# Performance work log

Measured on AMD Instinct MI355X. Metric: run time of the kernel, lower is better.

## Reference

```python
import jax, jax.numpy as jnp
import numpy as np

B, S, D, H = 4, 1024, 1024, 16
DH = D // H
EPS = 1e-5


def setup_inputs() -> dict:
    key = jax.random.key(0)
    ks = jax.random.split(key, 8)
    return {
        "q": jax.random.normal(ks[0], (B, S, D), jnp.float32),
        "k": jax.random.normal(ks[1], (B, S, D), jnp.float32),
        "v": jax.random.normal(ks[2], (B, S, D), jnp.float32),
        "mask": jnp.ones((B, S), jnp.float32),
        "scores": jax.random.normal(ks[3], (B, H, S, S), jnp.float32),
        "W_proj": jax.random.normal(ks[4], (D, D), jnp.float32) / np.sqrt(D),
        "W_minus": jax.random.normal(ks[5], (D, 2 * D), jnp.float32) / np.sqrt(2 * D),
        "ln_w": jnp.ones((D,), jnp.float32),
        "ln_b": jnp.zeros((D,), jnp.float32),
        "c": jnp.zeros((1,), jnp.float32),
    }


def reference(q, k, v, mask, scores, W_proj, W_minus, ln_w, ln_b, c):
    # split heads: (B,S,D) -> (B,S,H,DH)
    qh = q.reshape(B, S, H, DH)
    kh = k.reshape(B, S, H, DH)
    vh = v.reshape(B, S, H, DH)
    # scaled QK^T plus learnable-scaled residual scores
    att_scores = jnp.einsum("bqhd,bkhd->bhqk", qh, kh) / np.sqrt(DH) + c[0] * scores
    # additive mask (mask is (B, kv_len))
    att_scores = att_scores - 1e8 * (1.0 - mask)[:, None, None, :]
    att = jax.nn.softmax(att_scores, axis=-1)
    ctx = jnp.einsum("bhqk,bkhd->bqhd", att, vh).reshape(B, S, D)
    # proj (bias-free linear); dropout is identity at inference
    x = ctx @ W_proj.T
    # concat -> minus linear -> LayerNorm
    cat = jnp.concatenate([q, x], axis=-1)
    y = cat @ W_minus.T
    mu = jnp.mean(y, axis=-1, keepdims=True)
    var = jnp.mean((y - mu) ** 2, axis=-1, keepdims=True)
    y = (y - mu) * jax.lax.rsqrt(var + EPS) * ln_w + ln_b
    return (y, att_scores)
```

## Files before the change

### kernel.cpp

```cpp
#include <hip/hip_runtime.h>
#include <hip/hip_bf16.h>
#include <math.h>

#define BB 4
#define SS 1024
#define DD 1024
#define HH 16
#define DHH 64
#define BHH (BB * HH)

#define LDB 88
#define LDC 68

typedef __attribute__((ext_vector_type(8))) short short8;
typedef __attribute__((ext_vector_type(4))) float f32x4;

__device__ __forceinline__ unsigned short f2bf(float x) {
  __hip_bfloat16 h = __float2bfloat16(x);
  return *reinterpret_cast<unsigned short*>(&h);
}

__device__ __forceinline__ void stageb(const unsigned short* __restrict__ src, int ld,
                                       unsigned short* __restrict__ dst, int tid) {
#pragma unroll
  for (int u = 0; u < 2; ++u) {
    int cidx = tid + 256 * u;
    int r = cidx >> 3;
    int c8 = (cidx & 7) * 8;
    float4 v = *reinterpret_cast<const float4*>(src + (size_t)r * ld + c8);
    *reinterpret_cast<float4*>(dst + r * LDB + c8) = v;
  }
}

__device__ __forceinline__ short8 ldfrag(const unsigned short* __restrict__ base,
                                         int row16, int kh, int lane) {
  const unsigned short* p = base + (size_t)(row16 + (lane & 15)) * LDB + kh + (lane >> 4) * 8;
  return *reinterpret_cast<const short8*>(p);
}

__device__ __forceinline__ void mfma_tile(const unsigned short* As, const unsigned short* Bs,
                                          int w, int lane, f32x4 acc[4]) {
#pragma unroll
  for (int kh = 0; kh < 64; kh += 32) {
    short8 b = ldfrag(Bs, w * 16, kh, lane);
#pragma unroll
    for (int mb = 0; mb < 4; ++mb) {
      short8 a = ldfrag(As, mb * 16, kh, lane);
      acc[mb] = __builtin_amdgcn_mfma_f32_16x16x32_bf16(a, b, acc[mb], 0, 0, 0);
    }
  }
}

__device__ __forceinline__ void acc_to_lds(float* Cs, const f32x4 acc[4], int w, int lane,
                                           float scale) {
  int quad = lane >> 4, col = w * 16 + (lane & 15);
#pragma unroll
  for (int mb = 0; mb < 4; ++mb)
#pragma unroll
    for (int r = 0; r < 4; ++r)
      Cs[(mb * 16 + quad * 4 + r) * LDC + col] = acc[mb][r] * scale;
}

__global__ __launch_bounds__(256) void cvt_kernel(const float* __restrict__ in,
                                                  unsigned short* __restrict__ out, int n4) {
  int i = blockIdx.x * 256 + threadIdx.x;
  if (i < n4) {
    float4 v = reinterpret_cast<const float4*>(in)[i];
    ushort4 o;
    o.x = f2bf(v.x); o.y = f2bf(v.y); o.z = f2bf(v.z); o.w = f2bf(v.w);
    reinterpret_cast<ushort4*>(out)[i] = o;
  }
}

__global__ __launch_bounds__(256) void vtrans_kernel(const float* __restrict__ v,
                                                     unsigned short* __restrict__ vT) {
  __shared__ unsigned short T[64 * LDC];
  int tid = threadIdx.x;
  int s0 = blockIdx.x * 64, bh = blockIdx.y;
  int b = bh >> 4, h = bh & 15;
#pragma unroll
  for (int u = 0; u < 4; ++u) {
    int f = tid + 256 * u;
    int r = f >> 4, c4 = (f & 15) * 4;
    float4 vv = *reinterpret_cast<const float4*>(v + ((size_t)(b * SS + s0 + r)) * DD + h * DHH + c4);
    T[(c4 + 0) * LDC + r] = f2bf(vv.x);
    T[(c4 + 1) * LDC + r] = f2bf(vv.y);
    T[(c4 + 2) * LDC + r] = f2bf(vv.z);
    T[(c4 + 3) * LDC + r] = f2bf(vv.w);
  }
  __syncthreads();
#pragma unroll
  for (int u = 0; u < 4; ++u) {
    int f = tid + 256 * u;
    int d = f >> 4, s4 = (f & 15) * 4;
    ushort4 o = *reinterpret_cast<const ushort4*>(&T[d * LDC + s4]);
    *reinterpret_cast<ushort4*>(vT + ((size_t)(bh * DHH + d)) * SS + s0 + s4) = o;
  }
}

__global__ __launch_bounds__(256) void qk_mfma_kernel(
    const unsigned short* __restrict__ qb, const unsigned short* __restrict__ kb,
    const float* __restrict__ scores, const float* __restrict__ mask,
    const float* __restrict__ c, float* __restrict__ att,
    float* __restrict__ pmax, float* __restrict__ psum) {
  __shared__ unsigned short smem[2 * 64 * LDB];
  unsigned short* As = smem;
  unsigned short* Bs = smem + 64 * LDB;
  float* Cs = reinterpret_cast<float*>(smem);
  int tid = threadIdx.x, lane = tid & 63, w = tid >> 6;
  int kt = blockIdx.x, qt = blockIdx.y, bh = blockIdx.z;
  int b = bh >> 4, h = bh & 15;
  int qr0 = qt * 64, kr0 = kt * 64;

  stageb(qb + ((size_t)(b * SS + qr0)) * DD + h * DHH, DD, As, tid);
  stageb(kb + ((size_t)(b * SS + kr0)) * DD + h * DHH, DD, Bs, tid);
  __syncthreads();
  f32x4 acc[4] = {};
  mfma_tile(As, Bs, w, lane, acc);
  __syncthreads();
  acc_to_lds(Cs, acc, w, lane, 0.125f);
  __syncthreads();

  float cc = c[0];
#pragma unroll
  for (int u = 0; u < 4; ++u) {
    int f = tid + 256 * u;
    int row = f >> 4, c4 = (f & 15) * 4;
    int rg = bh * SS + qr0 + row;
    size_t goff = (size_t)rg * SS + kr0 + c4;
    float4 qk = *reinterpret_cast<const float4*>(&Cs[row * LDC + c4]);
    float4 sc = *reinterpret_cast<const float4*>(scores + goff);
    float4 mv = *reinterpret_cast<const float4*>(mask + b * SS + kr0 + c4);
    float o0 = qk.x + cc * sc.x - 1e8f * (1.0f - mv.x);
    float o1 = qk.y + cc * sc.y - 1e8f * (1.0f - mv.y);
    float o2 = qk.z + cc * sc.z - 1e8f * (1.0f - mv.z);
    float o3 = qk.w + cc * sc.w - 1e8f * (1.0f - mv.w);
    float4 ov = {o0, o1, o2, o3};
    *reinterpret_cast<float4*>(att + goff) = ov;
    float m = fmaxf(fmaxf(o0, o1), fmaxf(o2, o3));
#pragma unroll
    for (int off = 1; off <= 8; off <<= 1) m = fmaxf(m, __shfl_xor(m, off));
    float l = __expf(o0 - m) + __expf(o1 - m) + __expf(o2 - m) + __expf(o3 - m);
#pragma unroll
    for (int off = 1; off <= 8; off <<= 1) l += __shfl_xor(l, off);
    if ((tid & 15) == 0) {
      pmax[(size_t)rg * 16 + kt] = m;
      psum[(size_t)rg * 16 + kt] = l;
    }
  }
}

__global__ __launch_bounds__(256) void stats_reduce_kernel(
    const float* __restrict__ pmax, const float* __restrict__ psum,
    float* __restrict__ rowm, float* __restrict__ rowinvl) {
  int idx = blockIdx.x * 256 + threadIdx.x;
  const float* pm = pmax + (size_t)idx * 16;
  const float* pl = psum + (size_t)idx * 16;
  float m = pm[0], l = pl[0];
#pragma unroll
  for (int t = 1; t < 16; ++t) {
    float m2 = pm[t], l2 = pl[t];
    float nm = fmaxf(m, m2);
    l = l * __expf(m - nm) + l2 * __expf(m2 - nm);
    m = nm;
  }
  rowm[idx] = m;
  rowinvl[idx] = 1.0f / l;
}

__global__ __launch_bounds__(256) void ctx_mfma_kernel(
    const float* __restrict__ att, const unsigned short* __restrict__ vT,
    const float* __restrict__ rowm, const float* __restrict__ rowinvl,
    unsigned short* __restrict__ ctxb) {
  __shared__ unsigned short smem[2 * 64 * LDB];
  unsigned short* As = smem;
  unsigned short* Bs = smem + 64 * LDB;
  float* Cs = reinterpret_cast<float*>(smem);
  int tid = threadIdx.x, lane = tid & 63, w = tid >> 6;
  int qt = blockIdx.x, bh = blockIdx.y;
  int b = bh >> 4, h = bh & 15;
  int qr0 = qt * 64;
  f32x4 acc[4] = {};
  for (int kc = 0; kc < SS; kc += 64) {
#pragma unroll
    for (int u = 0; u < 4; ++u) {
      int f = tid + 256 * u;
      int row = f >> 4, c4 = (f & 15) * 4;
      int rg = bh * SS + qr0 + row;
      float4 s = *reinterpret_cast<const float4*>(att + (size_t)rg * SS + kc + c4);
      float mr = rowm[rg], il = rowinvl[rg];
      ushort4 pv;
      pv.x = f2bf(__expf(s.x - mr) * il);
      pv.y = f2bf(__expf(s.y - mr) * il);
      pv.z = f2bf(__expf(s.z - mr) * il);
      pv.w = f2bf(__expf(s.w - mr) * il);
      *reinterpret_cast<ushort4*>(&As[row * LDB + c4]) = pv;
    }
    stageb(vT + (size_t)bh * DHH * SS + kc, SS, Bs, tid);
    __syncthreads();
    mfma_tile(As, Bs, w, lane, acc);
    __syncthreads();
  }
  acc_to_lds(Cs, acc, w, lane, 1.0f);
  __syncthreads();
#pragma unroll
  for (int u = 0; u < 4; ++u) {
    int f = tid + 256 * u;
    int row = f >> 4, c4 = (f & 15) * 4;
    float4 vv = *reinterpret_cast<const float4*>(&Cs[row * LDC + c4]);
    ushort4 o;
    o.x = f2bf(vv.x); o.y = f2bf(vv.y); o.z = f2bf(vv.z); o.w = f2bf(vv.w);
    *reinterpret_cast<ushort4*>(ctxb + ((size_t)(b * SS + qr0 + row)) * DD + h * DHH + c4) = o;
  }
}

__global__ __launch_bounds__(256) void proj_mfma_kernel(
    const unsigned short* __restrict__ A, const unsigned short* __restrict__ W,
    unsigned short* __restrict__ X) {
  __shared__ unsigned short smem[2 * 64 * LDB];
  unsigned short* As = smem;
  unsigned short* Bs = smem + 64 * LDB;
  float* Cs = reinterpret_cast<float*>(smem);
  int tid = threadIdx.x, lane = tid & 63, w = tid >> 6;
  int d0 = blockIdx.x * 64, n0 = blockIdx.y * 64;
  f32x4 acc[4] = {};
  for (int kc = 0; kc < DD; kc += 64) {
    stageb(A + (size_t)n0 * DD + kc, DD, As, tid);
    stageb(W + (size_t)d0 * DD + kc, DD, Bs, tid);
    __syncthreads();
    mfma_tile(As, Bs, w, lane, acc);
    __syncthreads();
  }
  acc_to_lds(Cs, acc, w, lane, 1.0f);
  __syncthreads();
#pragma unroll
  for (int u = 0; u < 4; ++u) {
    int f = tid + 256 * u;
    int row = f >> 4, c4 = (f & 15) * 4;
    float4 vv = *reinterpret_cast<const float4*>(&Cs[row * LDC + c4]);
    ushort4 o;
    o.x = f2bf(vv.x); o.y = f2bf(vv.y); o.z = f2bf(vv.z); o.w = f2bf(vv.w);
    *reinterpret_cast<ushort4*>(X + (size_t)(n0 + row) * DD + d0 + c4) = o;
  }
}

__global__ __launch_bounds__(256) void minus_mfma_kernel(
    const unsigned short* __restrict__ qb, const unsigned short* __restrict__ xb,
    const unsigned short* __restrict__ Wm, float* __restrict__ Y) {
  __shared__ unsigned short smem[2 * 64 * LDB];
  unsigned short* As = smem;
  unsigned short* Bs = smem + 64 * LDB;
  float* Cs = reinterpret_cast<float*>(smem);
  int tid = threadIdx.x, lane = tid & 63, w = tid >> 6;
  int d0 = blockIdx.x * 64, n0 = blockIdx.y * 64;
  f32x4 acc[4] = {};
  for (int kc = 0; kc < 2 * DD; kc += 64) {
    const unsigned short* asrc = (kc < DD) ? (qb + (size_t)n0 * DD + kc)
                                           : (xb + (size_t)n0 * DD + (kc - DD));
    stageb(asrc, DD, As, tid);
    stageb(Wm + (size_t)d0 * (2 * DD) + kc, 2 * DD, Bs, tid);
    __syncthreads();
    mfma_tile(As, Bs, w, lane, acc);
    __syncthreads();
  }
  acc_to_lds(Cs, acc, w, lane, 1.0f);
  __syncthreads();
#pragma unroll
  for (int u = 0; u < 4; ++u) {
    int f = tid + 256 * u;
    int row = f >> 4, c4 = (f & 15) * 4;
    float4 vv = *reinterpret_cast<const float4*>(&Cs[row * LDC + c4]);
    *reinterpret_cast<float4*>(Y + (size_t)(n0 + row) * DD + d0 + c4) = vv;
  }
}

__global__ __launch_bounds__(256) void ln_kernel(
    float* __restrict__ Y, const float* __restrict__ w, const float* __restrict__ b) {
  __shared__ float ps[4], ps2[4];
  int row = blockIdx.x, t = threadIdx.x;
  float* rp = Y + (size_t)row * DD;
  float4 v = *reinterpret_cast<const float4*>(rp + t * 4);
  float s = v.x + v.y + v.z + v.w;
  float s2 = v.x * v.x + v.y * v.y + v.z * v.z + v.w * v.w;
#pragma unroll
  for (int o = 32; o > 0; o >>= 1) {
    s += __shfl_down(s, o);
    s2 += __shfl_down(s2, o);
  }
  if ((t & 63) == 0) { ps[t >> 6] = s; ps2[t >> 6] = s2; }
  __syncthreads();
  s = ps[0] + ps[1] + ps[2] + ps[3];
  s2 = ps2[0] + ps2[1] + ps2[2] + ps2[3];
  float mu = s * (1.0f / DD);
  float var = s2 * (1.0f / DD) - mu * mu;
  float rs = rsqrtf(var + 1e-5f);
  float4 wv = *reinterpret_cast<const float4*>(w + t * 4);
  float4 bv = *reinterpret_cast<const float4*>(b + t * 4);
  float4 ov;
  ov.x = (v.x - mu) * rs * wv.x + bv.x;
  ov.y = (v.y - mu) * rs * wv.y + bv.y;
  ov.z = (v.z - mu) * rs * wv.z + bv.z;
  ov.w = (v.w - mu) * rs * wv.w + bv.w;
  *reinterpret_cast<float4*>(rp + t * 4) = ov;
}

extern "C" void kernel_launch(void* const* d_in, const int* in_sizes, int n_in,
                              void* d_out, int out_size, void* d_ws, size_t ws_size,
                              hipStream_t stream) {
  const float* q      = (const float*)d_in[0];
  const float* k      = (const float*)d_in[1];
  const float* v      = (const float*)d_in[2];
  const float* mask   = (const float*)d_in[3];
  const float* scores = (const float*)d_in[4];
  const float* W_proj = (const float*)d_in[5];
  const float* W_minus= (const float*)d_in[6];
  const float* ln_w   = (const float*)d_in[7];
  const float* ln_b   = (const float*)d_in[8];
  const float* c      = (const float*)d_in[9];

  float* y   = (float*)d_out;
  float* att = y + (size_t)BB * SS * DD;

  const size_t MB = 1u << 20;
  char* w = (char*)d_ws;
  unsigned short* qb   = (unsigned short*)(w);
  unsigned short* kb   = (unsigned short*)(w + 8 * MB);
  unsigned short* vT   = (unsigned short*)(w + 16 * MB);
  unsigned short* Wpb  = (unsigned short*)(w + 24 * MB);
  unsigned short* Wmb  = (unsigned short*)(w + 26 * MB);
  unsigned short* ctxb = (unsigned short*)(w + 30 * MB);
  unsigned short* xb   = (unsigned short*)(w + 38 * MB);
  float* pmax    = (float*)(w + 46 * MB);
  float* psum    = (float*)(w + 50 * MB);
  float* rowm    = (float*)(w + 54 * MB);
  float* rowinvl = (float*)(w + 54 * MB + 256 * 1024);

  const int NQ = BB * SS * DD;
  cvt_kernel<<<dim3(NQ / 4 / 256), 256, 0, stream>>>(q, qb, NQ / 4);
  cvt_kernel<<<dim3(NQ / 4 / 256), 256, 0, stream>>>(k, kb, NQ / 4);
  cvt_kernel<<<dim3(DD * DD / 4 / 256), 256, 0, stream>>>(W_proj, Wpb, DD * DD / 4);
  cvt_kernel<<<dim3(2 * DD * DD / 4 / 256), 256, 0, stream>>>(W_minus, Wmb, 2 * DD * DD / 4);
  vtrans_kernel<<<dim3(16, BHH), 256, 0, stream>>>(v, vT);

  qk_mfma_kernel<<<dim3(16, 16, BHH), 256, 0, stream>>>(qb, kb, scores, mask, c, att, pmax, psum);
  stats_reduce_kernel<<<dim3(256), 256, 0, stream>>>(pmax, psum, rowm, rowinvl);
  ctx_mfma_kernel<<<dim3(16, BHH), 256, 0, stream>>>(att, vT, rowm, rowinvl, ctxb);
  proj_mfma_kernel<<<dim3(16, 64), 256, 0, stream>>>(ctxb, Wpb, xb);
  minus_mfma_kernel<<<dim3(16, 64), 256, 0, stream>>>(qb, xb, Wmb, y);
  ln_kernel<<<dim3(BB * SS), 256, 0, stream>>>(y, ln_w, ln_b);
}
```

Baseline: 735.7 us.

## Fuse QK scores, online softmax and PV into one flash-style attention kernel

```diff
diff --git a/kernel.cpp b/kernel.cpp
--- a/kernel.cpp
+++ b/kernel.cpp
@@ -98,110 +98,110 @@
   }
 }
 
-__global__ __launch_bounds__(256) void qk_mfma_kernel(
+__global__ __launch_bounds__(256) void attn_fused_kernel(
     const unsigned short* __restrict__ qb, const unsigned short* __restrict__ kb,
-    const float* __restrict__ scores, const float* __restrict__ mask,
-    const float* __restrict__ c, float* __restrict__ att,
-    float* __restrict__ pmax, float* __restrict__ psum) {
-  __shared__ unsigned short smem[2 * 64 * LDB];
-  unsigned short* As = smem;
-  unsigned short* Bs = smem + 64 * LDB;
-  float* Cs = reinterpret_cast<float*>(smem);
-  int tid = threadIdx.x, lane = tid & 63, w = tid >> 6;
-  int kt = blockIdx.x, qt = blockIdx.y, bh = blockIdx.z;
-  int b = bh >> 4, h = bh & 15;
-  int qr0 = qt * 64, kr0 = kt * 64;
-
-  stageb(qb + ((size_t)(b * SS + qr0)) * DD + h * DHH, DD, As, tid);
-  stageb(kb + ((size_t)(b * SS + kr0)) * DD + h * DHH, DD, Bs, tid);
-  __syncthreads();
-  f32x4 acc[4] = {};
-  mfma_tile(As, Bs, w, lane, acc);
-  __syncthreads();
-  acc_to_lds(Cs, acc, w, lane, 0.125f);
-  __syncthreads();
-
-  float cc = c[0];
-#pragma unroll
-  for (int u = 0; u < 4; ++u) {
-    int f = tid + 256 * u;
-    int row = f >> 4, c4 = (f & 15) * 4;
-    int rg = bh * SS + qr0 + row;
-    size_t goff = (size_t)rg * SS + kr0 + c4;
-    float4 qk = *reinterpret_cast<const float4*>(&Cs[row * LDC + c4]);
-    float4 sc = *reinterpret_cast<const float4*>(scores + goff);
-    float4 mv = *reinterpret_cast<const float4*>(mask + b * SS + kr0 + c4);
-    float o0 = qk.x + cc * sc.x - 1e8f * (1.0f - mv.x);
-    float o1 = qk.y + cc * sc.y - 1e8f * (1.0f - mv.y);
-    float o2 = qk.z + cc * sc.z - 1e8f * (1.0f - mv.z);
-    float o3 = qk.w + cc * sc.w - 1e8f * (1.0f - mv.w);
-    float4 ov = {o0, o1, o2, o3};
-    *reinterpret_cast<float4*>(att + goff) = ov;
-    float m = fmaxf(fmaxf(o0, o1), fmaxf(o2, o3));
-#pragma unroll
-    for (int off = 1; off <= 8; off <<= 1) m = fmaxf(m, __shfl_xor(m, off));
-    float l = __expf(o0 - m) + __expf(o1 - m) + __expf(o2 - m) + __expf(o3 - m);
-#pragma unroll
-    for (int off = 1; off <= 8; off <<= 1) l += __shfl_xor(l, off);
-    if ((tid & 15) == 0) {
-      pmax[(size_t)rg * 16 + kt] = m;
-      psum[(size_t)rg * 16 + kt] = l;
-    }
-  }
-}
-
-__global__ __launch_bounds__(256) void stats_reduce_kernel(
-    const float* __restrict__ pmax, const float* __restrict__ psum,
-    float* __restrict__ rowm, float* __restrict__ rowinvl) {
-  int idx = blockIdx.x * 256 + threadIdx.x;
-  const float* pm = pmax + (size_t)idx * 16;
-  const float* pl = psum + (size_t)idx * 16;
-  float m = pm[0], l = pl[0];
-#pragma unroll
-  for (int t = 1; t < 16; ++t) {
-    float m2 = pm[t], l2 = pl[t];
-    float nm = fmaxf(m, m2);
-    l = l * __expf(m - nm) + l2 * __expf(m2 - nm);
-    m = nm;
-  }
-  rowm[idx] = m;
-  rowinvl[idx] = 1.0f / l;
-}
-
-__global__ __launch_bounds__(256) void ctx_mfma_kernel(
-    const float* __restrict__ att, const unsigned short* __restrict__ vT,
-    const float* __restrict__ rowm, const float* __restrict__ rowinvl,
-    unsigned short* __restrict__ ctxb) {
-  __shared__ unsigned short smem[2 * 64 * LDB];
-  unsigned short* As = smem;
-  unsigned short* Bs = smem + 64 * LDB;
-  float* Cs = reinterpret_cast<float*>(smem);
+    const unsigned short* __restrict__ vT, const float* __restrict__ scores,
+    const float* __restrict__ mask, const float* __restrict__ c,
+    float* __restrict__ att, unsigned short* __restrict__ ctxb) {
+  __shared__ unsigned short Ps[64 * LDB];
+  __shared__ unsigned short Ks[64 * LDB];
+  __shared__ unsigned short Vs[64 * LDB];
+  __shared__ float Cs[64 * LDC];
+  __shared__ float mrun[64], lrun[64], ascale[64];
   int tid = threadIdx.x, lane = tid & 63, w = tid >> 6;
   int qt = blockIdx.x, bh = blockIdx.y;
   int b = bh >> 4, h = bh & 15;
   int qr0 = qt * 64;
-  f32x4 acc[4] = {};
-  for (int kc = 0; kc < SS; kc += 64) {
+
+  stageb(qb + ((size_t)(b * SS + qr0)) * DD + h * DHH, DD, Ps, tid);
+  if (tid < 64) { mrun[tid] = -3.0e38f; lrun[tid] = 0.0f; }
+  __syncthreads();
+
+  short8 qa[2][4];
+#pragma unroll
+  for (int kh = 0; kh < 2; ++kh)
+#pragma unroll
+    for (int mb = 0; mb < 4; ++mb)
+      qa[kh][mb] = ldfrag(Ps, mb * 16, kh * 32, lane);
+
+  float cc = c[0];
+  f32x4 accO[4] = {};
+
+  for (int kt = 0; kt < 16; ++kt) {
+    int kr0 = kt * 64;
+    stageb(kb + ((size_t)(b * SS + kr0)) * DD + h * DHH, DD, Ks, tid);
+    stageb(vT + (size_t)bh * DHH * SS + kr0, SS, Vs, tid);
+    __syncthreads();
+
+    f32x4 acc[4] = {};
+#pragma unroll
+    for (int kh = 0; kh < 2; ++kh) {
+      short8 bfr = ldfrag(Ks, w * 16, kh * 32, lane);
+#pragma unroll
+      for (int mb = 0; mb < 4; ++mb)
+        acc[mb] = __builtin_amdgcn_mfma_f32_16x16x32_bf16(qa[kh][mb], bfr, acc[mb], 0, 0, 0);
+    }
+    acc_to_lds(Cs, acc, w, lane, 0.125f);
+    __syncthreads();
+
 #pragma unroll
     for (int u = 0; u < 4; ++u) {
       int f = tid + 256 * u;
       int row = f >> 4, c4 = (f & 15) * 4;
       int rg = bh * SS + qr0 + row;
-      float4 s = *reinterpret_cast<const float4*>(att + (size_t)rg * SS + kc + c4);
-      float mr = rowm[rg], il = rowinvl[rg];
+      size_t goff = (size_t)rg * SS + kr0 + c4;
+      float4 qk = *reinterpret_cast<const float4*>(&Cs[row * LDC + c4]);
+      float4 sc = *reinterpret_cast<const float4*>(scores + goff);
+      float4 mv = *reinterpret_cast<const float4*>(mask + b * SS + kr0 + c4);
+      float o0 = qk.x + cc * sc.x - 1e8f * (1.0f - mv.x);
+      float o1 = qk.y + cc * sc.y - 1e8f * (1.0f - mv.y);
+      float o2 = qk.z + cc * sc.z - 1e8f * (1.0f - mv.z);
+      float o3 = qk.w + cc * sc.w - 1e8f * (1.0f - mv.w);
+      float4 ov = {o0, o1, o2, o3};
+      *reinterpret_cast<float4*>(att + goff) = ov;
+      float m = fmaxf(fmaxf(o0, o1), fmaxf(o2, o3));
+#pragma unroll
+      for (int off = 1; off <= 8; off <<= 1) m = fmaxf(m, __shfl_xor(m, off));
+      float mo = mrun[row];
+      float mn = fmaxf(mo, m);
+      float e0 = __expf(o0 - mn), e1 = __expf(o1 - mn);
+      float e2 = __expf(o2 - mn), e3 = __expf(o3 - mn);
+      float l = e0 + e1 + e2 + e3;
+#pragma unroll
+      for (int off = 1; off <= 8; off <<= 1) l += __shfl_xor(l, off);
       ushort4 pv;
-      pv.x = f2bf(__expf(s.x - mr) * il);
-      pv.y = f2bf(__expf(s.y - mr) * il);
-      pv.z = f2bf(__expf(s.z - mr) * il);
-      pv.w = f2bf(__expf(s.w - mr) * il);
-      *reinterpret_cast<ushort4*>(&As[row * LDB + c4]) = pv;
+      pv.x = f2bf(e0); pv.y = f2bf(e1); pv.z = f2bf(e2); pv.w = f2bf(e3);
+      *reinterpret_cast<ushort4*>(&Ps[row * LDB + c4]) = pv;
+      if ((tid & 15) == 0) {
+        float a = __expf(mo - mn);
+        lrun[row] = lrun[row] * a + l;
+        mrun[row] = mn;
+        ascale[row] = a;
+      }
     }
-    stageb(vT + (size_t)bh * DHH * SS + kc, SS, Bs, tid);
-    __syncthreads();
-    mfma_tile(As, Bs, w, lane, acc);
-    __syncthreads();
-  }
-  acc_to_lds(Cs, acc, w, lane, 1.0f);
+    __syncthreads();
+
+#pragma unroll
+    for (int mb = 0; mb < 4; ++mb) {
+      int rb = mb * 16 + (lane >> 4) * 4;
+      accO[mb][0] *= ascale[rb + 0];
+      accO[mb][1] *= ascale[rb + 1];
+      accO[mb][2] *= ascale[rb + 2];
+      accO[mb][3] *= ascale[rb + 3];
+    }
+    mfma_tile(Ps, Vs, w, lane, accO);
+    __syncthreads();
+  }
+
+#pragma unroll
+  for (int mb = 0; mb < 4; ++mb) {
+    int rb = mb * 16 + (lane >> 4) * 4;
+    accO[mb][0] *= 1.0f / lrun[rb + 0];
+    accO[mb][1] *= 1.0f / lrun[rb + 1];
+    accO[mb][2] *= 1.0f / lrun[rb + 2];
+    accO[mb][3] *= 1.0f / lrun[rb + 3];
+  }
+  acc_to_lds(Cs, accO, w, lane, 1.0f);
   __syncthreads();
 #pragma unroll
   for (int u = 0; u < 4; ++u) {
@@ -330,10 +330,6 @@
   unsigned short* Wmb  = (unsigned short*)(w + 26 * MB);
   unsigned short* ctxb = (unsigned short*)(w + 30 * MB);
   unsigned short* xb   = (unsigned short*)(w + 38 * MB);
-  float* pmax    = (float*)(w + 46 * MB);
-  float* psum    = (float*)(w + 50 * MB);
-  float* rowm    = (float*)(w + 54 * MB);
-  float* rowinvl = (float*)(w + 54 * MB + 256 * 1024);
 
   const int NQ = BB * SS * DD;
   cvt_kernel<<<dim3(NQ / 4 / 256), 256, 0, stream>>>(q, qb, NQ / 4);
@@ -342,9 +338,7 @@
   cvt_kernel<<<dim3(2 * DD * DD / 4 / 256), 256, 0, stream>>>(W_minus, Wmb, 2 * DD * DD / 4);
   vtrans_kernel<<<dim3(16, BHH), 256, 0, stream>>>(v, vT);
 
-  qk_mfma_kernel<<<dim3(16, 16, BHH), 256, 0, stream>>>(qb, kb, scores, mask, c, att, pmax, psum);
-  stats_reduce_kernel<<<dim3(256), 256, 0, stream>>>(pmax, psum, rowm, rowinvl);
-  ctx_mfma_kernel<<<dim3(16, BHH), 256, 0, stream>>>(att, vT, rowm, rowinvl, ctxb);
+  attn_fused_kernel<<<dim3(16, BHH), 256, 0, stream>>>(qb, kb, vT, scores, mask, c, att, ctxb);
   proj_mfma_kernel<<<dim3(16, 64), 256, 0, stream>>>(ctxb, Wpb, xb);
   minus_mfma_kernel<<<dim3(16, 64), 256, 0, stream>>>(qb, xb, Wmb, y);
   ln_kernel<<<dim3(BB * SS), 256, 0, stream>>>(y, ln_w, ln_b);
```

Result: slower. 761.1 us (+3.5%).
